# Optimization experiments

Measured on AMD Instinct MI355X. Metric: run time of the kernel, lower is better.

Reference implementation:

```python
import jax, jax.numpy as jnp
import numpy as np

N, C, H, W = 8, 256, 128, 128
HW = H * W
NB = 20            # boxes per image
TEMP = 0.5
RATIO = 1.0
IMG_H, IMG_W = 800.0, 800.0  # img_metas[i]['img_shape']


def setup_inputs() -> dict:
    key = jax.random.key(0)
    k1, k2, k3 = jax.random.split(key, 3)
    preds_S = jax.random.normal(k1, (HW, N, C), dtype=jnp.float32)
    preds_T = jax.random.normal(k2, (HW, N, C), dtype=jnp.float32)
    # boxes: random corner pairs in image coords, sorted so x1<=x2, y1<=y2
    u = jax.random.uniform(k3, (N, NB, 4), dtype=jnp.float32)
    x1 = jnp.minimum(u[..., 0], u[..., 2]) * IMG_W
    x2 = jnp.maximum(u[..., 0], u[..., 2]) * IMG_W
    y1 = jnp.minimum(u[..., 1], u[..., 3]) * IMG_H
    y2 = jnp.maximum(u[..., 1], u[..., 3]) * IMG_H
    gt_bboxes = jnp.stack([x1, y1, x2, y2], axis=-1)  # (N, NB, 4)
    return {"preds_S": preds_S, "preds_T": preds_T, "gt_bboxes": gt_bboxes}


def get_attention(preds, temp):
    # preds: (N, C, H, W)
    value = jnp.abs(preds)
    fea_map = value.mean(axis=1)                                   # (N, H, W)
    S_att = (H * W) * jax.nn.softmax((fea_map / temp).reshape(N, -1), axis=1)
    S_att = S_att.reshape(N, H, W)
    channel_map = value.mean(axis=(2, 3))                          # (N, C)
    C_att = C * jax.nn.softmax(channel_map / temp, axis=1)
    return S_att, C_att


def build_masks(gt_bboxes):
    # boxes scaled to feature grid (same math as torch loop, vectorized)
    wmin = jnp.floor(gt_bboxes[..., 0] / IMG_W * W).astype(jnp.int32)  # (N, NB)
    wmax = jnp.ceil(gt_bboxes[..., 2] / IMG_W * W).astype(jnp.int32)
    hmin = jnp.floor(gt_bboxes[..., 1] / IMG_H * H).astype(jnp.int32)
    hmax = jnp.ceil(gt_bboxes[..., 3] / IMG_H * H).astype(jnp.int32)
    area = 1.0 / (hmax + 1 - hmin).astype(jnp.float32) / (wmax + 1 - wmin).astype(jnp.float32)
    hh = jnp.arange(H)[None, None, :, None]
    ww = jnp.arange(W)[None, None, None, :]
    inside = ((hh >= hmin[:, :, None, None]) & (hh <= hmax[:, :, None, None]) &
              (ww >= wmin[:, :, None, None]) & (ww <= wmax[:, :, None, None]))  # (N, NB, H, W)
    # per-box max-scatter == max over boxes of (area where inside else 0)
    Mask_fg = jnp.max(jnp.where(inside, area[:, :, None, None], 0.0), axis=1)  # (N, H, W)
    Mask_bg = (Mask_fg <= 0).astype(jnp.float32)
    s = Mask_bg.sum(axis=(1, 2), keepdims=True)
    Mask_bg = jnp.where(s > 0, Mask_bg / s, Mask_bg)
    return Mask_fg, Mask_bg


def reference(preds_S, preds_T, gt_bboxes):
    # attention from DETACHED teacher features (preds_T.detach() in torch)
    pT_det = jax.lax.stop_gradient(preds_T)
    pT_new = pT_det.reshape(H, W, N, C).transpose(2, 3, 0, 1)  # (N, C, H, W)
    S_t, C_t = get_attention(pT_new, TEMP)

    Mask_fg, Mask_bg = build_masks(gt_bboxes)

    # flatten to the (HW, bs, .) layout of get_fea_loss
    flat = lambda m: m.transpose(1, 2, 0).reshape(HW, N, 1)
    S_t_f = flat(S_t)
    Mfg_f = flat(Mask_fg)
    Mbg_f = flat(Mask_bg)
    C_t_f = C_t[None]  # (1, bs, c) broadcast

    w = jnp.sqrt(S_t_f) * jnp.sqrt(C_t_f)
    fea_t = preds_T * w
    fea_s = preds_S * w
    diff = jnp.abs(fea_s - fea_t)
    fg_loss = jnp.sum(diff * jnp.sqrt(Mfg_f)) / HW
    bg_loss = jnp.sum(diff * jnp.sqrt(Mbg_f)) / HW
    return (fg_loss + bg_loss) * RATIO
```

## Files before the change

### kernel.cpp

```cpp
#include <hip/hip_runtime.h>

#define N_   8
#define C_   256
#define H_   128
#define W_   128
#define HW_  16384
#define NB_  20
constexpr float TEMP  = 0.5f;
constexpr float IMG_W = 800.0f;
constexpr float IMG_H = 800.0f;

__device__ __forceinline__ float waveReduceSum(float v) {
    v += __shfl_xor(v, 32, 64);
    v += __shfl_xor(v, 16, 64);
    v += __shfl_xor(v, 8, 64);
    v += __shfl_xor(v, 4, 64);
    v += __shfl_xor(v, 2, 64);
    v += __shfl_xor(v, 1, 64);
    return v;
}

__global__ __launch_bounds__(256) void k_stats(const float* __restrict__ pT,
                                               float* __restrict__ chan_sum,
                                               float* __restrict__ fea_sum) {
    const int n    = blockIdx.x & 7;
    const int p    = blockIdx.x >> 3;
    const int wave = threadIdx.x >> 6;
    const int lane = threadIdx.x & 63;
    float4 cacc = make_float4(0.f, 0.f, 0.f, 0.f);
    const int hw0 = p * 256 + wave * 64;
    for (int i = 0; i < 64; ++i) {
        const int hw = hw0 + i;
        const float4 v = *(const float4*)(pT + ((size_t)(hw * N_ + n)) * C_ + lane * 4);
        const float ax = fabsf(v.x), ay = fabsf(v.y), az = fabsf(v.z), aw = fabsf(v.w);
        cacc.x += ax; cacc.y += ay; cacc.z += az; cacc.w += aw;
        const float s = waveReduceSum(ax + ay + az + aw);
        if (lane == 0) fea_sum[n * HW_ + hw] = s;
    }
    __shared__ float lds[4][C_];
    lds[wave][lane * 4 + 0] = cacc.x;
    lds[wave][lane * 4 + 1] = cacc.y;
    lds[wave][lane * 4 + 2] = cacc.z;
    lds[wave][lane * 4 + 3] = cacc.w;
    __syncthreads();
    const int c = threadIdx.x;
    const float v = lds[0][c] + lds[1][c] + lds[2][c] + lds[3][c];
    atomicAdd(&chan_sum[n * C_ + c], v);
}

__global__ __launch_bounds__(256) void k_soft(const float* __restrict__ fea_sum,
                                              const float* __restrict__ chan_sum,
                                              float* __restrict__ stats,
                                              float* __restrict__ B) {
    const int n = blockIdx.x;
    const int tid = threadIdx.x;
    __shared__ float red[256];
    float m = -1e30f;
    for (int i = tid; i < HW_; i += 256) m = fmaxf(m, fea_sum[n * HW_ + i]);
    red[tid] = m; __syncthreads();
    for (int s = 128; s > 0; s >>= 1) { if (tid < s) red[tid] = fmaxf(red[tid], red[tid + s]); __syncthreads(); }
    const float smax = red[0] * (1.0f / (C_ * TEMP));
    __syncthreads();
    float acc = 0.f;
    for (int i = tid; i < HW_; i += 256)
        acc += expf(fea_sum[n * HW_ + i] * (1.0f / (C_ * TEMP)) - smax);
    red[tid] = acc; __syncthreads();
    for (int s = 128; s > 0; s >>= 1) { if (tid < s) red[tid] += red[tid + s]; __syncthreads(); }
    const float sden = red[0];
    __syncthreads();
    const float lc = chan_sum[n * C_ + tid] * (1.0f / (HW_ * TEMP));
    red[tid] = lc; __syncthreads();
    for (int s = 128; s > 0; s >>= 1) { if (tid < s) red[tid] = fmaxf(red[tid], red[tid + s]); __syncthreads(); }
    const float cmax = red[0]; __syncthreads();
    const float e = expf(lc - cmax);
    red[tid] = e; __syncthreads();
    for (int s = 128; s > 0; s >>= 1) { if (tid < s) red[tid] += red[tid + s]; __syncthreads(); }
    const float cden = red[0];
    B[n * C_ + tid] = sqrtf((float)C_ * e / cden);
    if (tid == 0) { stats[n] = smax; stats[N_ + n] = sden; }
}

__global__ __launch_bounds__(256) void k_mask(const float* __restrict__ gt,
                                              float* __restrict__ Mfg,
                                              float* __restrict__ bgcnt) {
    const int n = blockIdx.y;
    const int hw = blockIdx.x * 256 + threadIdx.x;
    const int h = hw >> 7, w = hw & 127;
    float fg = 0.f;
    for (int b = 0; b < NB_; ++b) {
        const float* bx = gt + ((size_t)n * NB_ + b) * 4;
        const float x1 = bx[0], y1 = bx[1], x2 = bx[2], y2 = bx[3];
        const int wmin = (int)floorf(x1 / IMG_W * (float)W_);
        const int wmax = (int)ceilf (x2 / IMG_W * (float)W_);
        const int hmin = (int)floorf(y1 / IMG_H * (float)H_);
        const int hmax = (int)ceilf (y2 / IMG_H * (float)H_);
        if (h >= hmin && h <= hmax && w >= wmin && w <= wmax) {
            const float area = 1.0f / (float)(hmax + 1 - hmin) / (float)(wmax + 1 - wmin);
            fg = fmaxf(fg, area);
        }
    }
    Mfg[n * HW_ + hw] = fg;
    __shared__ float red[256];
    red[threadIdx.x] = (fg <= 0.f) ? 1.f : 0.f;
    __syncthreads();
    for (int s = 128; s > 0; s >>= 1) { if (threadIdx.x < s) red[threadIdx.x] += red[threadIdx.x + s]; __syncthreads(); }
    if (threadIdx.x == 0) atomicAdd(&bgcnt[n], red[0]);
}

__global__ __launch_bounds__(256) void k_A(const float* __restrict__ fea_sum,
                                           const float* __restrict__ Mfg,
                                           const float* __restrict__ bgcnt,
                                           const float* __restrict__ stats,
                                           float* __restrict__ A) {
    const int n = blockIdx.y;
    const int hw = blockIdx.x * 256 + threadIdx.x;
    const float smax = stats[n], sden = stats[N_ + n];
    const float logit = fea_sum[n * HW_ + hw] * (1.0f / (C_ * TEMP));
    const float S_att = (float)HW_ * expf(logit - smax) / sden;
    const float fg = Mfg[n * HW_ + hw];
    const float s = bgcnt[n];
    const float bg = (fg <= 0.f) ? ((s > 0.f) ? 1.0f / s : 1.0f) : 0.f;
    A[n * HW_ + hw] = sqrtf(S_att) * (sqrtf(fg) + sqrtf(bg)) * (1.0f / (float)HW_);
}

__global__ __launch_bounds__(256) void k_main(const float* __restrict__ pS,
                                              const float* __restrict__ pT,
                                              const float* __restrict__ A,
                                              const float* __restrict__ B,
                                              float* __restrict__ partials) {
    const int wave = threadIdx.x >> 6, lane = threadIdx.x & 63;
    const int wg = blockIdx.x * 4 + wave;
    const int n = wg & 7;
    const int widx = wg >> 3;
    const float4 B4 = *(const float4*)(B + n * C_ + lane * 4);
    float acc = 0.f;
    const int hw0 = widx * 32;
    for (int i = 0; i < 32; ++i) {
        const int hw = hw0 + i;
        const size_t off = ((size_t)(hw * N_ + n)) * C_ + lane * 4;
        const float4 sv = *(const float4*)(pS + off);
        const float4 tv = *(const float4*)(pT + off);
        const float part = fabsf(sv.x - tv.x) * B4.x + fabsf(sv.y - tv.y) * B4.y +
                           fabsf(sv.z - tv.z) * B4.z + fabsf(sv.w - tv.w) * B4.w;
        acc += A[n * HW_ + hw] * part;
    }
    acc = waveReduceSum(acc);
    __shared__ float red[4];
    if (lane == 0) red[wave] = acc;
    __syncthreads();
    if (threadIdx.x == 0) partials[blockIdx.x] = red[0] + red[1] + red[2] + red[3];
}

__global__ __launch_bounds__(256) void k_final(const float* __restrict__ partials,
                                               float* __restrict__ out) {
    float a = 0.f;
    for (int i = threadIdx.x; i < 1024; i += 256) a += partials[i];
    __shared__ float red[256];
    red[threadIdx.x] = a; __syncthreads();
    for (int s = 128; s > 0; s >>= 1) { if (threadIdx.x < s) red[threadIdx.x] += red[threadIdx.x + s]; __syncthreads(); }
    if (threadIdx.x == 0) out[0] = red[0];
}

extern "C" void kernel_launch(void* const* d_in, const int* in_sizes, int n_in,
                              void* d_out, int out_size, void* d_ws, size_t ws_size,
                              hipStream_t stream) {
    const float* pS = (const float*)d_in[0];
    const float* pT = (const float*)d_in[1];
    const float* gt = (const float*)d_in[2];
    float* ws = (float*)d_ws;

    float* chan_sum = ws;
    float* bgcnt    = ws + 2048;
    float* stats    = ws + 2056;
    float* fea_sum  = ws + 4096;
    float* Mfg      = fea_sum + N_ * HW_;
    float* A        = Mfg + N_ * HW_;
    float* B        = A + N_ * HW_;
    float* partials = B + N_ * C_;

    hipMemsetAsync(ws, 0, 2056 * sizeof(float), stream);

    k_stats<<<512, 256, 0, stream>>>(pT, chan_sum, fea_sum);
    k_soft<<<N_, 256, 0, stream>>>(fea_sum, chan_sum, stats, B);
    k_mask<<<dim3(HW_ / 256, N_), 256, 0, stream>>>(gt, Mfg, bgcnt);
    k_A<<<dim3(HW_ / 256, N_), 256, 0, stream>>>(fea_sum, Mfg, bgcnt, stats, A);
    k_main<<<1024, 256, 0, stream>>>(pS, pT, A, B, partials);
    k_final<<<1, 256, 0, stream>>>(partials, (float*)d_out);
}
```

Before: 339.4 us.

## Fuse softmax, mask and weight kernels per image; use LDS transpose for row sums

```diff
diff --git a/kernel.cpp b/kernel.cpp
--- a/kernel.cpp
+++ b/kernel.cpp
@@ -10,16 +10,6 @@
 constexpr float IMG_W = 800.0f;
 constexpr float IMG_H = 800.0f;
 
-__device__ __forceinline__ float waveReduceSum(float v) {
-    v += __shfl_xor(v, 32, 64);
-    v += __shfl_xor(v, 16, 64);
-    v += __shfl_xor(v, 8, 64);
-    v += __shfl_xor(v, 4, 64);
-    v += __shfl_xor(v, 2, 64);
-    v += __shfl_xor(v, 1, 64);
-    return v;
-}
-
 __global__ __launch_bounds__(256) void k_stats(const float* __restrict__ pT,
                                                float* __restrict__ chan_sum,
                                                float* __restrict__ fea_sum) {
@@ -27,34 +17,71 @@
     const int p    = blockIdx.x >> 3;
     const int wave = threadIdx.x >> 6;
     const int lane = threadIdx.x & 63;
+    __shared__ float rowp[4][64 * 65];
+    __shared__ float chl[4][C_];
+
     float4 cacc = make_float4(0.f, 0.f, 0.f, 0.f);
     const int hw0 = p * 256 + wave * 64;
+    const float* base = pT + ((size_t)(hw0 * N_ + n)) * C_ + lane * 4;
+    #pragma unroll 8
     for (int i = 0; i < 64; ++i) {
-        const int hw = hw0 + i;
-        const float4 v = *(const float4*)(pT + ((size_t)(hw * N_ + n)) * C_ + lane * 4);
+        const float4 v = *(const float4*)(base + (size_t)i * (N_ * C_));
         const float ax = fabsf(v.x), ay = fabsf(v.y), az = fabsf(v.z), aw = fabsf(v.w);
         cacc.x += ax; cacc.y += ay; cacc.z += az; cacc.w += aw;
-        const float s = waveReduceSum(ax + ay + az + aw);
-        if (lane == 0) fea_sum[n * HW_ + hw] = s;
+        rowp[wave][i * 65 + lane] = ax + ay + az + aw;
     }
-    __shared__ float lds[4][C_];
-    lds[wave][lane * 4 + 0] = cacc.x;
-    lds[wave][lane * 4 + 1] = cacc.y;
-    lds[wave][lane * 4 + 2] = cacc.z;
-    lds[wave][lane * 4 + 3] = cacc.w;
+    chl[wave][lane * 4 + 0] = cacc.x;
+    chl[wave][lane * 4 + 1] = cacc.y;
+    chl[wave][lane * 4 + 2] = cacc.z;
+    chl[wave][lane * 4 + 3] = cacc.w;
     __syncthreads();
+    {
+        const int w_ = threadIdx.x >> 6, r = threadIdx.x & 63;
+        float s = 0.f;
+        #pragma unroll
+        for (int j = 0; j < 64; ++j) s += rowp[w_][r * 65 + j];
+        fea_sum[n * HW_ + p * 256 + threadIdx.x] = s;
+    }
     const int c = threadIdx.x;
-    const float v = lds[0][c] + lds[1][c] + lds[2][c] + lds[3][c];
-    atomicAdd(&chan_sum[n * C_ + c], v);
+    atomicAdd(&chan_sum[n * C_ + c], chl[0][c] + chl[1][c] + chl[2][c] + chl[3][c]);
 }
 
-__global__ __launch_bounds__(256) void k_soft(const float* __restrict__ fea_sum,
+__global__ __launch_bounds__(256) void k_perN(const float* __restrict__ fea_sum,
                                               const float* __restrict__ chan_sum,
-                                              float* __restrict__ stats,
+                                              const float* __restrict__ gt,
+                                              float* __restrict__ A,
                                               float* __restrict__ B) {
     const int n = blockIdx.x;
     const int tid = threadIdx.x;
     __shared__ float red[256];
+    __shared__ int   bh0[NB_], bh1[NB_], bw0[NB_], bw1[NB_];
+    __shared__ float barea[NB_];
+    __shared__ float MfgL[HW_];
+    __shared__ float sc[4];
+
+    if (tid < NB_) {
+        const float* bx = gt + ((size_t)n * NB_ + tid) * 4;
+        const float wminf = floorf(bx[0] / IMG_W * (float)W_);
+        const float wmaxf = ceilf (bx[2] / IMG_W * (float)W_);
+        const float hminf = floorf(bx[1] / IMG_H * (float)H_);
+        const float hmaxf = ceilf (bx[3] / IMG_H * (float)H_);
+        bw0[tid] = (int)wminf; bw1[tid] = (int)wmaxf;
+        bh0[tid] = (int)hminf; bh1[tid] = (int)hmaxf;
+        barea[tid] = 1.0f / (hmaxf + 1.0f - hminf) / (wmaxf + 1.0f - wminf);
+    }
+
+    const float lc = chan_sum[n * C_ + tid] * (1.0f / (HW_ * TEMP));
+    red[tid] = lc; __syncthreads();
+    for (int s = 128; s > 0; s >>= 1) { if (tid < s) red[tid] = fmaxf(red[tid], red[tid + s]); __syncthreads(); }
+    const float cmax = red[0]; __syncthreads();
+    const float e = expf(lc - cmax);
+    red[tid] = e; __syncthreads();
+    for (int s = 128; s > 0; s >>= 1) { if (tid < s) red[tid] += red[tid + s]; __syncthreads(); }
+    if (tid == 0) sc[0] = red[0];
+    __syncthreads();
+    B[n * C_ + tid] = sqrtf((float)C_ * e / sc[0]);
+
+    __syncthreads();
     float m = -1e30f;
     for (int i = tid; i < HW_; i += 256) m = fmaxf(m, fea_sum[n * HW_ + i]);
     red[tid] = m; __syncthreads();
@@ -68,59 +95,44 @@
     for (int s = 128; s > 0; s >>= 1) { if (tid < s) red[tid] += red[tid + s]; __syncthreads(); }
     const float sden = red[0];
     __syncthreads();
-    const float lc = chan_sum[n * C_ + tid] * (1.0f / (HW_ * TEMP));
-    red[tid] = lc; __syncthreads();
-    for (int s = 128; s > 0; s >>= 1) { if (tid < s) red[tid] = fmaxf(red[tid], red[tid + s]); __syncthreads(); }
-    const float cmax = red[0]; __syncthreads();
-    const float e = expf(lc - cmax);
-    red[tid] = e; __syncthreads();
+
+    const int w = tid & 127;
+    unsigned wmask = 0;
+    for (int b = 0; b < NB_; ++b)
+        if (w >= bw0[b] && w <= bw1[b]) wmask |= (1u << b);
+    float cnt = 0.f;
+    for (int k = 0; k < HW_ / 256; ++k) {
+        const int i = tid + k * 256;
+        const int h = i >> 7;
+        float fg = 0.f;
+        for (int b = 0; b < NB_; ++b)
+            if (((wmask >> b) & 1u) && h >= bh0[b] && h <= bh1[b]) fg = fmaxf(fg, barea[b]);
+        MfgL[i] = fg;
+        cnt += (fg <= 0.f) ? 1.f : 0.f;
+    }
+    red[tid] = cnt; __syncthreads();
     for (int s = 128; s > 0; s >>= 1) { if (tid < s) red[tid] += red[tid + s]; __syncthreads(); }
-    const float cden = red[0];
-    B[n * C_ + tid] = sqrtf((float)C_ * e / cden);
-    if (tid == 0) { stats[n] = smax; stats[N_ + n] = sden; }
+    const float bgsum = red[0];
+    const float bgval = (bgsum > 0.f) ? 1.0f / bgsum : 1.0f;
+
+    for (int k = 0; k < HW_ / 256; ++k) {
+        const int i = tid + k * 256;
+        const float fg = MfgL[i];
+        const float S_att = (float)HW_ *
+            expf(fea_sum[n * HW_ + i] * (1.0f / (C_ * TEMP)) - smax) / sden;
+        const float bgv = (fg <= 0.f) ? bgval : 0.f;
+        A[n * HW_ + i] = sqrtf(S_att) * (sqrtf(fg) + sqrtf(bgv)) * (1.0f / (float)HW_);
+    }
 }
 
-__global__ __launch_bounds__(256) void k_mask(const float* __restrict__ gt,
-                                              float* __restrict__ Mfg,
-                                              float* __restrict__ bgcnt) {
-    const int n = blockIdx.y;
-    const int hw = blockIdx.x * 256 + threadIdx.x;
-    const int h = hw >> 7, w = hw & 127;
-    float fg = 0.f;
-    for (int b = 0; b < NB_; ++b) {
-        const float* bx = gt + ((size_t)n * NB_ + b) * 4;
-        const float x1 = bx[0], y1 = bx[1], x2 = bx[2], y2 = bx[3];
-        const int wmin = (int)floorf(x1 / IMG_W * (float)W_);
-        const int wmax = (int)ceilf (x2 / IMG_W * (float)W_);
-        const int hmin = (int)floorf(y1 / IMG_H * (float)H_);
-        const int hmax = (int)ceilf (y2 / IMG_H * (float)H_);
-        if (h >= hmin && h <= hmax && w >= wmin && w <= wmax) {
-            const float area = 1.0f / (float)(hmax + 1 - hmin) / (float)(wmax + 1 - wmin);
-            fg = fmaxf(fg, area);
-        }
-    }
-    Mfg[n * HW_ + hw] = fg;
-    __shared__ float red[256];
-    red[threadIdx.x] = (fg <= 0.f) ? 1.f : 0.f;
-    __syncthreads();
-    for (int s = 128; s > 0; s >>= 1) { if (threadIdx.x < s) red[threadIdx.x] += red[threadIdx.x + s]; __syncthreads(); }
-    if (threadIdx.x == 0) atomicAdd(&bgcnt[n], red[0]);
-}
-
-__global__ __launch_bounds__(256) void k_A(const float* __restrict__ fea_sum,
-                                           const float* __restrict__ Mfg,
-                                           const float* __restrict__ bgcnt,
-                                           const float* __restrict__ stats,
-                                           float* __restrict__ A) {
-    const int n = blockIdx.y;
-    const int hw = blockIdx.x * 256 + threadIdx.x;
-    const float smax = stats[n], sden = stats[N_ + n];
-    const float logit = fea_sum[n * HW_ + hw] * (1.0f / (C_ * TEMP));
-    const float S_att = (float)HW_ * expf(logit - smax) / sden;
-    const float fg = Mfg[n * HW_ + hw];
-    const float s = bgcnt[n];
-    const float bg = (fg <= 0.f) ? ((s > 0.f) ? 1.0f / s : 1.0f) : 0.f;
-    A[n * HW_ + hw] = sqrtf(S_att) * (sqrtf(fg) + sqrtf(bg)) * (1.0f / (float)HW_);
+__device__ __forceinline__ float waveReduceSum(float v) {
+    v += __shfl_xor(v, 32, 64);
+    v += __shfl_xor(v, 16, 64);
+    v += __shfl_xor(v, 8, 64);
+    v += __shfl_xor(v, 4, 64);
+    v += __shfl_xor(v, 2, 64);
+    v += __shfl_xor(v, 1, 64);
+    return v;
 }
 
 __global__ __launch_bounds__(256) void k_main(const float* __restrict__ pS,
@@ -135,6 +147,7 @@
     const float4 B4 = *(const float4*)(B + n * C_ + lane * 4);
     float acc = 0.f;
     const int hw0 = widx * 32;
+    #pragma unroll 4
     for (int i = 0; i < 32; ++i) {
         const int hw = hw0 + i;
         const size_t off = ((size_t)(hw * N_ + n)) * C_ + lane * 4;
@@ -170,20 +183,15 @@
     float* ws = (float*)d_ws;
 
     float* chan_sum = ws;
-    float* bgcnt    = ws + 2048;
-    float* stats    = ws + 2056;
-    float* fea_sum  = ws + 4096;
-    float* Mfg      = fea_sum + N_ * HW_;
-    float* A        = Mfg + N_ * HW_;
+    float* fea_sum  = ws + 2048;
+    float* A        = fea_sum + N_ * HW_;
     float* B        = A + N_ * HW_;
     float* partials = B + N_ * C_;
 
-    hipMemsetAsync(ws, 0, 2056 * sizeof(float), stream);
+    hipMemsetAsync(chan_sum, 0, 2048 * sizeof(float), stream);
 
     k_stats<<<512, 256, 0, stream>>>(pT, chan_sum, fea_sum);
-    k_soft<<<N_, 256, 0, stream>>>(fea_sum, chan_sum, stats, B);
-    k_mask<<<dim3(HW_ / 256, N_), 256, 0, stream>>>(gt, Mfg, bgcnt);
-    k_A<<<dim3(HW_ / 256, N_), 256, 0, stream>>>(fea_sum, Mfg, bgcnt, stats, A);
+    k_perN<<<N_, 256, 0, stream>>>(fea_sum, chan_sum, gt, A, B);
     k_main<<<1024, 256, 0, stream>>>(pS, pT, A, B, partials);
     k_final<<<1, 256, 0, stream>>>(partials, (float*)d_out);
 }
```

New measurement: 344.5 us. Within noise of the previous version (+1.5%).
